# Kernel tuning notes

Hardware: AMD Instinct MI355X
Metric: run time of the kernel (lower is better)

## Reference

```python
import jax, jax.numpy as jnp
import numpy as np

N_NODES = 100000
N_EDGES = 400000
N_GRAPHS = 4096
BN_EPS = 1e-5


def _glorot(key, shape):
    fan_in, fan_out = shape
    lim = np.sqrt(6.0 / (fan_in + fan_out))
    return jax.random.uniform(key, shape, jnp.float32, -lim, lim)


def setup_inputs() -> dict:
    key = jax.random.key(0)
    ks = jax.random.split(key, 16)
    x = jax.random.normal(ks[0], (N_NODES, 373), jnp.float32)
    edge_index = jax.random.randint(ks[1], (2, N_EDGES), 0, N_NODES, jnp.int64)
    batch = jnp.sort(jax.random.randint(ks[2], (N_NODES,), 0, N_GRAPHS, jnp.int64))
    params = {
        # GIN layer 1 MLP: 373->256->256
        'W1a': _glorot(ks[3], (373, 256)), 'b1a': jnp.zeros((256,), jnp.float32),
        'W1b': _glorot(ks[4], (256, 256)), 'b1b': jnp.zeros((256,), jnp.float32),
        'g1': jnp.ones((256,), jnp.float32), 'be1': jnp.zeros((256,), jnp.float32),
        # GIN layer 2 MLP: 256->128->128
        'W2a': _glorot(ks[5], (256, 128)), 'b2a': jnp.zeros((128,), jnp.float32),
        'W2b': _glorot(ks[6], (128, 128)), 'b2b': jnp.zeros((128,), jnp.float32),
        'g2': jnp.ones((128,), jnp.float32), 'be2': jnp.zeros((128,), jnp.float32),
        # GIN layer 3 MLP: 128->64->64
        'W3a': _glorot(ks[7], (128, 64)), 'b3a': jnp.zeros((64,), jnp.float32),
        'W3b': _glorot(ks[8], (64, 64)), 'b3b': jnp.zeros((64,), jnp.float32),
        'g3': jnp.ones((64,), jnp.float32), 'be3': jnp.zeros((64,), jnp.float32),
        # head
        'Wf1': _glorot(ks[9], (64, 16)), 'bf1': jnp.zeros((16,), jnp.float32),
        'Wf2': _glorot(ks[10], (16, 1)), 'bf2': jnp.zeros((1,), jnp.float32),
    }
    return {'x': x, 'edge_index': edge_index, 'batch': batch, **params}


def _gin_conv(x, src, dst, Wa, ba, Wb, bb):
    # sum-aggregate neighbor messages (eps = 0 default in GINConv)
    agg = jax.ops.segment_sum(x[src], dst, num_segments=N_NODES)
    h = x + agg
    h = jax.nn.relu(h @ Wa + ba) @ Wb + bb
    return h


def _batchnorm(x, gamma, beta):
    mu = jnp.mean(x, axis=0)
    var = jnp.var(x, axis=0)
    return (x - mu) * jax.lax.rsqrt(var + BN_EPS) * gamma + beta


def reference(x, edge_index, batch,
              W1a, b1a, W1b, b1b, g1, be1,
              W2a, b2a, W2b, b2b, g2, be2,
              W3a, b3a, W3b, b3b, g3, be3,
              Wf1, bf1, Wf2, bf2):
    src, dst = edge_index[0], edge_index[1]
    h = jax.nn.relu(_gin_conv(x, src, dst, W1a, b1a, W1b, b1b))
    h = _batchnorm(h, g1, be1)
    h = jax.nn.relu(_gin_conv(h, src, dst, W2a, b2a, W2b, b2b))
    h = _batchnorm(h, g2, be2)
    h = jax.nn.relu(_gin_conv(h, src, dst, W3a, b3a, W3b, b3b))
    h = _batchnorm(h, g3, be3)
    # global_add_pool: [N, 64] -> [G, 64]
    pooled = jax.ops.segment_sum(h, batch, num_segments=N_GRAPHS)
    out = jax.nn.relu(pooled @ Wf1 + bf1)
    # dropout omitted (eval mode)
    out = jax.nn.relu(out @ Wf2 + bf2)
    return out.reshape(-1)
```

## Files before the change

### kernel.cpp

```cpp
#include <hip/hip_runtime.h>

#define N_NODES 100000
#define N_EDGES 400000
#define N_GRAPHS 4096
#define BN_EPS 1e-5f
#define DEG_CAP 96

typedef unsigned short ushort_t;
typedef short short8 __attribute__((ext_vector_type(8)));
typedef unsigned short ushort4v __attribute__((ext_vector_type(4)));
typedef unsigned short ushort8v __attribute__((ext_vector_type(8)));
typedef float floatx4 __attribute__((ext_vector_type(4)));

__device__ __forceinline__ ushort_t f2b(float f) {
    union { float f; unsigned u; } v; v.f = f;
    unsigned r = v.u + 0x7fffu + ((v.u >> 16) & 1u);
    return (ushort_t)(r >> 16);
}
__device__ __forceinline__ float b2f(ushort_t b) {
    union { unsigned u; float f; } v; v.u = ((unsigned)b) << 16;
    return v.f;
}

__global__ void k_pad_x(const float* __restrict__ x, ushort_t* __restrict__ xb,
                        int* __restrict__ cursor,
                        const float* __restrict__ W1a, ushort_t* __restrict__ BT1) {
    int t = threadIdx.x;
    if (blockIdx.x >= N_NODES) {
        int b = blockIdx.x - N_NODES;
        int n = b / 3, kc = b % 3;
        int k = kc * 128 + t;
        float v = (k < 373) ? W1a[(long)k * 256 + n] : 0.f;
        BT1[(long)n * 384 + k] = f2b(v);
        return;
    }
    int n = blockIdx.x;
    const float* xr = x + (long)n * 373;
    ushort_t* o = xb + (long)n * 384;
    if (t < 93) {
        float v0 = xr[t * 4 + 0], v1 = xr[t * 4 + 1], v2 = xr[t * 4 + 2], v3 = xr[t * 4 + 3];
        ushort4v s = {f2b(v0), f2b(v1), f2b(v2), f2b(v3)};
        *(ushort4v*)(o + t * 4) = s;
    } else if (t == 93) {
        o[372] = f2b(xr[372]);
        o[373] = 0; o[374] = 0; o[375] = 0;
    } else if (t == 94 || t == 95) {
        ushort4v z = {0, 0, 0, 0};
        *(ushort4v*)(o + 376 + (t - 94) * 4) = z;
    } else if (t == 96) {
        cursor[n] = 0;
    }
}

__global__ void k_fill(const int* __restrict__ src, const int* __restrict__ dst,
                       int* __restrict__ cursor, int* __restrict__ elist) {
    int e = blockIdx.x * blockDim.x + threadIdx.x;
    if (e < N_EDGES) {
        int d = dst[e];
        int slot = atomicAdd(&cursor[d], 1);
        if (slot < DEG_CAP) elist[(long)d * DEG_CAP + slot] = src[e];
    }
}

__global__ void k_prep_scaled(const float* __restrict__ W, const float* __restrict__ scsh,
                              ushort_t* __restrict__ BT, float* __restrict__ biasE,
                              int K, int Kp, int Nn) {
    int n = blockIdx.y;
    int k = blockIdx.x * 128 + threadIdx.x;
    if (k < Kp) {
        float v = (k < K) ? W[(long)k * Nn + n] * scsh[k] : 0.f;
        BT[(long)n * Kp + k] = f2b(v);
    }
    if (blockIdx.x == 0) {
        __shared__ float red[2];
        float s = 0.f;
        for (int kk = threadIdx.x; kk < K; kk += 128) s += scsh[K + kk] * W[(long)kk * Nn + n];
#pragma unroll
        for (int off = 32; off >= 1; off >>= 1) s += __shfl_xor(s, off);
        if ((threadIdx.x & 63) == 0) red[threadIdx.x >> 6] = s;
        __syncthreads();
        if (threadIdx.x == 0) biasE[n] = red[0] + red[1];
    }
}

template<int KP, int TN, bool STATS>
__global__ __launch_bounds__(256) void k_gemm(const ushort_t* __restrict__ A,
                                              const ushort_t* __restrict__ BT,
                                              const float* __restrict__ bias,
                                              ushort_t* __restrict__ C,
                                              float* __restrict__ partials,
                                              int M, int Nn, int relu) {
    __shared__ __align__(16) ushort_t As[128 * 32];
    __shared__ __align__(16) ushort_t Bs[TN * 32];
    __shared__ float swred[STATS ? 4 * 2 * TN : 1];
    const int tid = threadIdx.x;
    const int wave = tid >> 6, lane = tid & 63;
    const int ln = lane & 15, kg = lane >> 4;
    const long rowBase = (long)blockIdx.y * 128;
    const int colBase = blockIdx.x * TN;

    constexpr int RT = (TN == 128) ? 4 : 2;
    const int rowOff = (TN == 128) ? ((wave >> 1) * 64) : (wave * 32);
    const int colOff = (TN == 128) ? ((wave & 1) * 64) : 0;

    const ushort_t* aSrc[2];
#pragma unroll
    for (int i = 0; i < 2; i++) {
        long r = rowBase + i * 64 + (tid >> 2);
        if (r >= M) r = M - 1;
        aSrc[i] = A + r * KP + (tid & 3) * 8;
    }
    const ushort_t* bSrc[TN / 64];
#pragma unroll
    for (int i = 0; i < TN / 64; i++) {
        long cc = colBase + i * 64 + (tid >> 2);
        bSrc[i] = BT + cc * KP + (tid & 3) * 8;
    }
    ushort_t* aDst = As + wave * 512;
    ushort_t* bDst = Bs + wave * 512;

    floatx4 acc[RT][4];
#pragma unroll
    for (int i = 0; i < RT; i++)
#pragma unroll
        for (int j = 0; j < 4; j++) acc[i][j] = (floatx4){0.f, 0.f, 0.f, 0.f};

    for (int k0 = 0; k0 < KP; k0 += 32) {
        __syncthreads();
#pragma unroll
        for (int i = 0; i < 2; i++)
            __builtin_amdgcn_global_load_lds(
                (const __attribute__((address_space(1))) void*)(aSrc[i] + k0),
                (__attribute__((address_space(3))) void*)(aDst + i * 2048), 16, 0, 0);
#pragma unroll
        for (int i = 0; i < TN / 64; i++)
            __builtin_amdgcn_global_load_lds(
                (const __attribute__((address_space(1))) void*)(bSrc[i] + k0),
                (__attribute__((address_space(3))) void*)(bDst + i * 2048), 16, 0, 0);
        __syncthreads();

        short8 afr[RT], bfr[4];
#pragma unroll
        for (int rt = 0; rt < RT; rt++)
            afr[rt] = *(const short8*)&As[(rowOff + rt * 16 + ln) * 32 + kg * 8];
#pragma unroll
        for (int tn = 0; tn < 4; tn++)
            bfr[tn] = *(const short8*)&Bs[(colOff + tn * 16 + ln) * 32 + kg * 8];
#pragma unroll
        for (int rt = 0; rt < RT; rt++)
#pragma unroll
            for (int tn = 0; tn < 4; tn++)
                acc[rt][tn] = __builtin_amdgcn_mfma_f32_16x16x32_bf16(afr[rt], bfr[tn], acc[rt][tn], 0, 0, 0);
    }

    if constexpr (STATS) {
        for (int i = tid; i < 4 * 2 * TN; i += 256) swred[i] = 0.f;
        __syncthreads();
    }

    float sums[4] = {0.f, 0.f, 0.f, 0.f};
    float sqs[4]  = {0.f, 0.f, 0.f, 0.f};
#pragma unroll
    for (int rt = 0; rt < RT; rt++) {
#pragma unroll
        for (int tn = 0; tn < 4; tn++) {
            int gc = colBase + colOff + tn * 16 + ln;
            float bv = bias ? bias[gc] : 0.f;
#pragma unroll
            for (int r = 0; r < 4; r++) {
                long gr = rowBase + rowOff + rt * 16 + kg * 4 + r;
                if (gr < M) {
                    float v = acc[rt][tn][r] + bv;
                    if (relu) v = fmaxf(v, 0.f);
                    ushort_t sb = f2b(v);
                    C[gr * Nn + gc] = sb;
                    if (STATS) {
                        float vb = b2f(sb);
                        sums[tn] += vb;
                        sqs[tn] += vb * vb;
                    }
                }
            }
        }
    }
    if constexpr (STATS) {
#pragma unroll
        for (int tn = 0; tn < 4; tn++) {
            float s = sums[tn], q = sqs[tn];
            s += __shfl_xor(s, 16); q += __shfl_xor(q, 16);
            s += __shfl_xor(s, 32); q += __shfl_xor(q, 32);
            if (kg == 0) {
                int c = colOff + tn * 16 + ln;
                swred[wave * 2 * TN + c] = s;
                swred[wave * 2 * TN + TN + c] = q;
            }
        }
        __syncthreads();
        const int by = blockIdx.y;
        const int gyd = gridDim.y;
        for (int c = tid; c < TN; c += 256) {
            float ssum = 0.f, ssq = 0.f;
#pragma unroll
            for (int w = 0; w < 4; w++) {
                ssum += swred[w * 2 * TN + c];
                ssq  += swred[w * 2 * TN + TN + c];
            }
            long gc = colBase + c;
            partials[gc * gyd + by] = ssum;
            partials[((long)Nn + gc) * gyd + by] = ssq;
        }
    }
}

template<int KP, int TN>
__global__ __launch_bounds__(256, 4) void k_gemm_agg(const ushort_t* __restrict__ y,
                                                  const int* __restrict__ cursor,
                                                  const int* __restrict__ elist,
                                                  const float* __restrict__ badd,
                                                  const ushort_t* __restrict__ BT,
                                                  const float* __restrict__ bias,
                                                  ushort_t* __restrict__ C,
                                                  float* __restrict__ partials,
                                                  int M, int Nn) {
    __shared__ __align__(16) ushort_t Af[128 * KP];
    __shared__ __align__(16) ushort_t Bs[TN * 32];
    float* swred = (float*)Af;
    const int tid = threadIdx.x;
    const int wave = tid >> 6, lane = tid & 63;
    const int ln = lane & 15, kg = lane >> 4;
    const long rowBase = (long)blockIdx.y * 128;
    constexpr int CPR = KP / 8;
    constexpr int TPR = CPR;
    constexpr int RPS = 256 / TPR;

    {
        const int lr = tid / TPR;
        const int ck = tid % TPR;
        const int c0 = ck * 8;
        float bd[8];
#pragma unroll
        for (int j = 0; j < 8; j++) bd[j] = badd[c0 + j];
        for (int s = 0; s < 128; s += RPS) {
            int r = s + lr;
            long gr = rowBase + r; if (gr >= M) gr = M - 1;
            int cnt = cursor[gr]; if (cnt > DEG_CAP) cnt = DEG_CAP;
            const int* el = elist + gr * DEG_CAP;
            int4 e0 = *(const int4*)el;
            int4 e1 = *(const int4*)(el + 4);
            int ids[8] = {e0.x, e0.y, e0.z, e0.w, e1.x, e1.y, e1.z, e1.w};
            ushort8v sv = *(const ushort8v*)(y + gr * KP + c0);
            ushort8v rr[8];
#pragma unroll
            for (int i = 0; i < 8; i++)
                if (i < cnt) rr[i] = *(const ushort8v*)(y + (long)ids[i] * KP + c0);
            float av[8];
#pragma unroll
            for (int j = 0; j < 8; j++) av[j] = b2f(sv[j]);
#pragma unroll
            for (int i = 0; i < 8; i++)
                if (i < cnt) {
#pragma unroll
                    for (int j = 0; j < 8; j++) av[j] += b2f(rr[i][j]);
                }
            for (int i = 8; i < cnt; i++) {
                ushort8v u = *(const ushort8v*)(y + (long)el[i] * KP + c0);
#pragma unroll
                for (int j = 0; j < 8; j++) av[j] += b2f(u[j]);
            }
            ushort8v ov;
#pragma unroll
            for (int j = 0; j < 8; j++) ov[j] = f2b(fmaxf(av[j] + bd[j], 0.f));
            int cks = ck ^ (r & (CPR - 1));
            *(ushort8v*)&Af[r * KP + cks * 8] = ov;
        }
    }

    constexpr int RT = (TN == 128) ? 4 : 2;
    const int rowOff = (TN == 128) ? ((wave >> 1) * 64) : (wave * 32);
    const int colOff = (TN == 128) ? ((wave & 1) * 64) : 0;
    const ushort_t* bSrc[TN / 64];
#pragma unroll
    for (int i = 0; i < TN / 64; i++) {
        long cc = i * 64 + (tid >> 2);
        bSrc[i] = BT + cc * KP + (tid & 3) * 8;
    }
    ushort_t* bDst = Bs + wave * 512;

    floatx4 acc[RT][4];
#pragma unroll
    for (int i = 0; i < RT; i++)
#pragma unroll
        for (int j = 0; j < 4; j++) acc[i][j] = (floatx4){0.f, 0.f, 0.f, 0.f};

    for (int k0 = 0; k0 < KP; k0 += 32) {
        __syncthreads();
#pragma unroll
        for (int i = 0; i < TN / 64; i++)
            __builtin_amdgcn_global_load_lds(
                (const __attribute__((address_space(1))) void*)(bSrc[i] + k0),
                (__attribute__((address_space(3))) void*)(bDst + i * 2048), 16, 0, 0);
        __syncthreads();

        short8 afr[RT], bfr[4];
#pragma unroll
        for (int rt = 0; rt < RT; rt++) {
            int row = rowOff + rt * 16 + ln;
            int cks = ((k0 >> 3) + kg) ^ (row & (CPR - 1));
            afr[rt] = *(const short8*)&Af[row * KP + cks * 8];
        }
#pragma unroll
        for (int tn = 0; tn < 4; tn++)
            bfr[tn] = *(const short8*)&Bs[(colOff + tn * 16 + ln) * 32 + kg * 8];
#pragma unroll
        for (int rt = 0; rt < RT; rt++)
#pragma unroll
            for (int tn = 0; tn < 4; tn++)
                acc[rt][tn] = __builtin_amdgcn_mfma_f32_16x16x32_bf16(afr[rt], bfr[tn], acc[rt][tn], 0, 0, 0);
    }

    __syncthreads();
    for (int i = tid; i < 4 * 2 * TN; i += 256) swred[i] = 0.f;
    __syncthreads();

    float sums[4] = {0.f, 0.f, 0.f, 0.f};
    float sqs[4]  = {0.f, 0.f, 0.f, 0.f};
#pragma unroll
    for (int rt = 0; rt < RT; rt++) {
#pragma unroll
        for (int tn = 0; tn < 4; tn++) {
            int gc = colOff + tn * 16 + ln;
            float bv = bias[gc];
#pragma unroll
            for (int r = 0; r < 4; r++) {
                long gr = rowBase + rowOff + rt * 16 + kg * 4 + r;
                if (gr < M) {
                    float v = fmaxf(acc[rt][tn][r] + bv, 0.f);
                    ushort_t sb = f2b(v);
                    C[gr * Nn + gc] = sb;
                    float vb = b2f(sb);
                    sums[tn] += vb;
                    sqs[tn] += vb * vb;
                }
            }
        }
    }
#pragma unroll
    for (int tn = 0; tn < 4; tn++) {
        float s = sums[tn], q = sqs[tn];
        s += __shfl_xor(s, 16); q += __shfl_xor(q, 16);
        s += __shfl_xor(s, 32); q += __shfl_xor(q, 32);
        if (kg == 0) {
            int c = colOff + tn * 16 + ln;
            swred[wave * 2 * TN + c] = s;
            swred[wave * 2 * TN + TN + c] = q;
        }
    }
    __syncthreads();
    const int by = blockIdx.y;
    const int gyd = gridDim.y;
    for (int c = tid; c < TN; c += 256) {
        float ssum = 0.f, ssq = 0.f;
#pragma unroll
        for (int w = 0; w < 4; w++) {
            ssum += swred[w * 2 * TN + c];
            ssq  += swred[w * 2 * TN + TN + c];
        }
        partials[(long)c * gyd + by] = ssum;
        partials[((long)Nn + c) * gyd + by] = ssq;
    }
}

template<int D>
__global__ void k_aggregate(const ushort_t* __restrict__ y, const int* __restrict__ cursor,
                            const int* __restrict__ elist, const float* __restrict__ badd,
                            ushort_t* __restrict__ out, int nblk,
                            const float* __restrict__ Wn, ushort_t* __restrict__ BTn,
                            int KWn, int NWn) {
    int t = threadIdx.x;
    if ((int)blockIdx.x >= nblk) {
        int b = blockIdx.x - nblk;
        int nk = KWn >> 6;
        int n = b / nk, kc = b - n * nk;
        int k = kc * 64 + t;
        BTn[(long)n * KWn + k] = f2b(Wn[(long)k * NWn + n]);
        return;
    }
    const int CG = D / 4;
    const int NPB = 64 / CG;
    int n = blockIdx.x * NPB + t / CG;
    int c = (t % CG) * 4;
    if (n >= N_NODES) return;
    int cnt = cursor[n];
    if (cnt > DEG_CAP) cnt = DEG_CAP;
    const int* el = elist + (long)n * DEG_CAP;
    int4 e0 = *(const int4*)el;
    int4 e1 = *(const int4*)(el + 4);
    int ids[8] = {e0.x, e0.y, e0.z, e0.w, e1.x, e1.y, e1.z, e1.w};
    ushort4v sv = *(const ushort4v*)(y + (long)n * D + c);
    ushort4v rr[8];
#pragma unroll
    for (int i = 0; i < 8; i++)
        if (i < cnt) rr[i] = *(const ushort4v*)(y + (long)ids[i] * D + c);
    float t0 = b2f(sv.x), t1 = b2f(sv.y), t2 = b2f(sv.z), t3 = b2f(sv.w);
#pragma unroll
    for (int i = 0; i < 8; i++)
        if (i < cnt) {
            t0 += b2f(rr[i].x); t1 += b2f(rr[i].y); t2 += b2f(rr[i].z); t3 += b2f(rr[i].w);
        }
    for (int i = 8; i < cnt; i++) {
        ushort4v u = *(const ushort4v*)(y + (long)el[i] * D + c);
        t0 += b2f(u.x); t1 += b2f(u.y); t2 += b2f(u.z); t3 += b2f(u.w);
    }
    t0 = fmaxf(t0 + badd[c + 0], 0.f);
    t1 = fmaxf(t1 + badd[c + 1], 0.f);
    t2 = fmaxf(t2 + badd[c + 2], 0.f);
    t3 = fmaxf(t3 + badd[c + 3], 0.f);
    ushort4v o = {f2b(t0), f2b(t1), f2b(t2), f2b(t3)};
    *(ushort4v*)(out + (long)n * D + c) = o;
}

__global__ void k_bn(const float* __restrict__ partials, int gy,
                     const float* __restrict__ gamma, const float* __restrict__ beta,
                     float* __restrict__ scsh, int K,
                     const float* __restrict__ Wn, ushort_t* __restrict__ BTn,
                     int KWn, int NWn) {
    int b = blockIdx.x;
    int t = threadIdx.x;
    if (b >= K) {
        int p = b - K;
        int nk = KWn >> 6;
        int n = p / nk, kc = p - n * nk;
        int k = kc * 64 + t;
        BTn[(long)n * KWn + k] = f2b(Wn[(long)k * NWn + n]);
        return;
    }
    const float* ps = partials + (long)b * gy;
    const float* pq = partials + (long)(K + b) * gy;
    float s = 0.f, q = 0.f;
    for (int i = t; i < gy; i += 64) { s += ps[i]; q += pq[i]; }
#pragma unroll
    for (int off = 32; off >= 1; off >>= 1) { s += __shfl_xor(s, off); q += __shfl_xor(q, off); }
    if (t == 0) {
        float invN = 1.0f / (float)N_NODES;
        float mu = s * invN;
        float var = fmaxf(q * invN - mu * mu, 0.f);
        float sc = rsqrtf(var + BN_EPS) * gamma[b];
        scsh[b] = sc;
        scsh[K + b] = beta[b] - mu * sc;
    }
}

__global__ void k_poolhead(const ushort_t* __restrict__ h, const int* __restrict__ batch,
                           const float* __restrict__ scsh,
                           const float* __restrict__ Wf1, const float* __restrict__ bf1,
                           const float* __restrict__ Wf2, const float* __restrict__ bf2,
                           float* __restrict__ out) {
    __shared__ float pl[64];
    __shared__ float hid[16];
    int g = blockIdx.x;
    int c = threadIdx.x;
    int lo = 0, hi = N_NODES;
    while (lo < hi) { int mid = (lo + hi) >> 1; if (batch[mid] < g) lo = mid + 1; else hi = mid; }
    int start = lo;
    hi = N_NODES;
    while (lo < hi) { int mid = (lo + hi) >> 1; if (batch[mid] < g + 1) lo = mid + 1; else hi = mid; }
    int end = lo;
    float s = 0.f;
    for (int r = start; r < end; r++) s += b2f(h[(long)r * 64 + c]);
    pl[c] = s * scsh[c] + scsh[64 + c] * (float)(end - start);
    __syncthreads();
    if (c < 16) {
        float sh = bf1[c];
        for (int j = 0; j < 64; j++) sh += pl[j] * Wf1[j * 16 + c];
        hid[c] = fmaxf(sh, 0.f);
    }
    __syncthreads();
    if (c == 0) {
        float o = bf2[0];
#pragma unroll
        for (int k = 0; k < 16; k++) o += hid[k] * Wf2[k];
        out[g] = fmaxf(o, 0.f);
    }
}

extern "C" void kernel_launch(void* const* d_in, const int* in_sizes, int n_in,
                              void* d_out, int out_size, void* d_ws, size_t ws_size,
                              hipStream_t stream) {
    const float* x    = (const float*)d_in[0];
    const int*  ei    = (const int*)d_in[1];
    const int*  batch = (const int*)d_in[2];
    const float* W1a = (const float*)d_in[3];
    const float* b1a = (const float*)d_in[4];
    const float* W1b = (const float*)d_in[5];
    const float* b1b = (const float*)d_in[6];
    const float* g1  = (const float*)d_in[7];
    const float* be1 = (const float*)d_in[8];
    const float* W2a = (const float*)d_in[9];
    const float* b2a = (const float*)d_in[10];
    const float* W2b = (const float*)d_in[11];
    const float* b2b = (const float*)d_in[12];
    const float* g2  = (const float*)d_in[13];
    const float* be2 = (const float*)d_in[14];
    const float* W3a = (const float*)d_in[15];
    const float* b3a = (const float*)d_in[16];
    const float* W3b = (const float*)d_in[17];
    const float* b3b = (const float*)d_in[18];
    const float* g3  = (const float*)d_in[19];
    const float* be3 = (const float*)d_in[20];
    const float* Wf1 = (const float*)d_in[21];
    const float* bf1 = (const float*)d_in[22];
    const float* Wf2 = (const float*)d_in[23];
    const float* bf2 = (const float*)d_in[24];

    const int N = N_NODES, E = N_EDGES;
    const int* src = ei;
    const int* dst = ei + E;
    const int gy = (N + 127) / 128;

    char* wp = (char*)d_ws;
    auto carve = [&](size_t bytes) {
        char* p = wp;
        wp += (bytes + 255) & ~(size_t)255;
        return (void*)p;
    };
    ushort_t* xb     = (ushort_t*)carve((size_t)N * 384 * 2);
    ushort_t* bufA   = (ushort_t*)carve((size_t)N * 256 * 2);
    ushort_t* bufB   = (ushort_t*)carve((size_t)N * 256 * 2);
    int*      elist  = (int*)carve((size_t)N * DEG_CAP * 4);
    int*      cursor = (int*)carve((size_t)N * 4);
    ushort_t* BT1    = (ushort_t*)carve((size_t)256 * 384 * 2);
    ushort_t* BT2    = (ushort_t*)carve((size_t)256 * 384 * 2);
    float*    scsh   = (float*)carve(512 * 4);
    float*    biasE  = (float*)carve(256 * 4);
    float*    partials = (float*)carve((size_t)2 * 256 * gy * 4);

    dim3 blk(256);

    k_pad_x<<<N + 768, 128, 0, stream>>>(x, xb, cursor, W1a, BT1);
    k_fill<<<(E + 255) / 256, blk, 0, stream>>>(src, dst, cursor, elist);

    k_gemm<384, 128, false><<<dim3(2, gy), blk, 0, stream>>>(xb, BT1, nullptr, bufA, nullptr, N, 256, 0);
    k_aggregate<256><<<N + 1024, 64, 0, stream>>>(bufA, cursor, elist, b1a, bufB, N, W1b, BT2, 256, 256);
    k_gemm<256, 128, true><<<dim3(2, gy), blk, 0, stream>>>(bufB, BT2, b1b, bufA, partials, N, 256, 1);
    k_bn<<<256 + 256, 64, 0, stream>>>(partials, gy, g1, be1, scsh, 256, W2b, BT2, 128, 128);

    k_prep_scaled<<<dim3(2, 128), 128, 0, stream>>>(W2a, scsh, BT1, biasE, 256, 256, 128);
    k_gemm<256, 128, false><<<dim3(1, gy), blk, 0, stream>>>(bufA, BT1, biasE, bufB, nullptr, N, 128, 0);
    k_gemm_agg<128, 128><<<dim3(1, gy), blk, 0, stream>>>(bufB, cursor, elist, b2a, BT2, b2b, bufA, partials, N, 128);
    k_bn<<<128 + 64, 64, 0, stream>>>(partials, gy, g2, be2, scsh, 128, W3b, BT2, 64, 64);

    k_prep_scaled<<<dim3(1, 64), 128, 0, stream>>>(W3a, scsh, BT1, biasE, 128, 128, 64);
    k_gemm<128, 64, false><<<dim3(1, gy), blk, 0, stream>>>(bufA, BT1, biasE, bufB, nullptr, N, 64, 0);
    k_gemm_agg<64, 64><<<dim3(1, gy), blk, 0, stream>>>(bufB, cursor, elist, b3a, BT2, b3b, bufA, partials, N, 64);
    k_bn<<<64, 64, 0, stream>>>(partials, gy, g3, be3, scsh, 64, nullptr, nullptr, 64, 64);

    k_poolhead<<<N_GRAPHS, 64, 0, stream>>>(bufA, batch, scsh, Wf1, bf1, Wf2, bf2, (float*)d_out);
}
```

Baseline: 627.4 us.

## Fuse fp32-to-bf16 conversion of x into first GEMM and widen N tile

Removes the separate padding/conversion pass that wrote a bf16 copy of x. The first GEMM now reads fp32 x directly, converts to bf16 into padded shared memory, and computes all 256 output columns per block. The layer-1 second GEMM also moves to a 256-wide tile so each A tile is loaded once instead of twice. This saves a full write and re-read of the converted input, but the A loads are now scalar, unaligned fp32 reads (row stride 373) done synchronously, and the larger accumulator arrays raise register pressure and may lower occupancy.

```diff
diff --git a/kernel.cpp b/kernel.cpp
--- a/kernel.cpp
+++ b/kernel.cpp
@@ -22,34 +22,20 @@
     return v.f;
 }
 
-__global__ void k_pad_x(const float* __restrict__ x, ushort_t* __restrict__ xb,
-                        int* __restrict__ cursor,
+__global__ void k_prep0(int* __restrict__ cursor,
                         const float* __restrict__ W1a, ushort_t* __restrict__ BT1) {
     int t = threadIdx.x;
-    if (blockIdx.x >= N_NODES) {
-        int b = blockIdx.x - N_NODES;
-        int n = b / 3, kc = b % 3;
-        int k = kc * 128 + t;
-        float v = (k < 373) ? W1a[(long)k * 256 + n] : 0.f;
-        BT1[(long)n * 384 + k] = f2b(v);
+    int b = blockIdx.x;
+    if (b < 782) {
+        int i = b * 128 + t;
+        if (i < N_NODES) cursor[i] = 0;
         return;
     }
-    int n = blockIdx.x;
-    const float* xr = x + (long)n * 373;
-    ushort_t* o = xb + (long)n * 384;
-    if (t < 93) {
-        float v0 = xr[t * 4 + 0], v1 = xr[t * 4 + 1], v2 = xr[t * 4 + 2], v3 = xr[t * 4 + 3];
-        ushort4v s = {f2b(v0), f2b(v1), f2b(v2), f2b(v3)};
-        *(ushort4v*)(o + t * 4) = s;
-    } else if (t == 93) {
-        o[372] = f2b(xr[372]);
-        o[373] = 0; o[374] = 0; o[375] = 0;
-    } else if (t == 94 || t == 95) {
-        ushort4v z = {0, 0, 0, 0};
-        *(ushort4v*)(o + 376 + (t - 94) * 4) = z;
-    } else if (t == 96) {
-        cursor[n] = 0;
-    }
+    b -= 782;
+    int n = b / 3, kc = b % 3;
+    int k = kc * 128 + t;
+    float v = (k < 373) ? W1a[(long)k * 256 + n] : 0.f;
+    BT1[(long)n * 384 + k] = f2b(v);
 }
 
 __global__ void k_fill(const int* __restrict__ src, const int* __restrict__ dst,
@@ -80,6 +66,87 @@
         if ((threadIdx.x & 63) == 0) red[threadIdx.x >> 6] = s;
         __syncthreads();
         if (threadIdx.x == 0) biasE[n] = red[0] + red[1];
+    }
+}
+
+__global__ __launch_bounds__(256) void k_gemm_x(const float* __restrict__ x,
+                                                const ushort_t* __restrict__ BT,
+                                                ushort_t* __restrict__ C, int M) {
+    __shared__ __align__(16) ushort_t As[128 * 40];
+    __shared__ __align__(16) ushort_t Bs[256 * 32];
+    const int tid = threadIdx.x;
+    const int wave = tid >> 6, lane = tid & 63;
+    const int ln = lane & 15, kg = lane >> 4;
+    const long rowBase = (long)blockIdx.x * 128;
+    const int rowOff = (wave >> 1) * 64;
+    const int colOff = (wave & 1) * 128;
+
+    const int sr = tid >> 1;
+    const int sc0 = (tid & 1) * 16;
+    long gr = rowBase + sr; if (gr >= M) gr = M - 1;
+    const float* xr = x + gr * 373;
+
+    const ushort_t* bSrc[4];
+#pragma unroll
+    for (int i = 0; i < 4; i++) {
+        long cc = i * 64 + (tid >> 2);
+        bSrc[i] = BT + cc * 384 + (tid & 3) * 8;
+    }
+    ushort_t* bDst = Bs + wave * 512;
+
+    floatx4 acc[4][8];
+#pragma unroll
+    for (int i = 0; i < 4; i++)
+#pragma unroll
+        for (int j = 0; j < 8; j++) acc[i][j] = (floatx4){0.f, 0.f, 0.f, 0.f};
+
+    for (int k0 = 0; k0 < 384; k0 += 32) {
+        __syncthreads();
+        ushort8v o0, o1;
+#pragma unroll
+        for (int j = 0; j < 8; j++) {
+            int c = k0 + sc0 + j;
+            o0[j] = f2b((c < 373) ? xr[c] : 0.f);
+        }
+#pragma unroll
+        for (int j = 0; j < 8; j++) {
+            int c = k0 + sc0 + 8 + j;
+            o1[j] = f2b((c < 373) ? xr[c] : 0.f);
+        }
+        *(ushort8v*)&As[sr * 40 + sc0] = o0;
+        *(ushort8v*)&As[sr * 40 + sc0 + 8] = o1;
+#pragma unroll
+        for (int i = 0; i < 4; i++)
+            __builtin_amdgcn_global_load_lds(
+                (const __attribute__((address_space(1))) void*)(bSrc[i] + k0),
+                (__attribute__((address_space(3))) void*)(bDst + i * 2048), 16, 0, 0);
+        __syncthreads();
+
+        short8 afr[4], bfr[8];
+#pragma unroll
+        for (int rt = 0; rt < 4; rt++)
+            afr[rt] = *(const short8*)&As[(rowOff + rt * 16 + ln) * 40 + kg * 8];
+#pragma unroll
+        for (int ct = 0; ct < 8; ct++)
+            bfr[ct] = *(const short8*)&Bs[(colOff + ct * 16 + ln) * 32 + kg * 8];
+#pragma unroll
+        for (int rt = 0; rt < 4; rt++)
+#pragma unroll
+            for (int ct = 0; ct < 8; ct++)
+                acc[rt][ct] = __builtin_amdgcn_mfma_f32_16x16x32_bf16(afr[rt], bfr[ct], acc[rt][ct], 0, 0, 0);
+    }
+
+#pragma unroll
+    for (int rt = 0; rt < 4; rt++) {
+#pragma unroll
+        for (int ct = 0; ct < 8; ct++) {
+            int gc = colOff + ct * 16 + ln;
+#pragma unroll
+            for (int r = 0; r < 4; r++) {
+                long g2 = rowBase + rowOff + rt * 16 + kg * 4 + r;
+                if (g2 < M) C[g2 * 256 + gc] = f2b(acc[rt][ct][r]);
+            }
+        }
     }
 }
 
@@ -99,9 +166,10 @@
     const long rowBase = (long)blockIdx.y * 128;
     const int colBase = blockIdx.x * TN;
 
-    constexpr int RT = (TN == 128) ? 4 : 2;
-    const int rowOff = (TN == 128) ? ((wave >> 1) * 64) : (wave * 32);
-    const int colOff = (TN == 128) ? ((wave & 1) * 64) : 0;
+    constexpr int RT = (TN == 64) ? 2 : 4;
+    constexpr int CT = (TN == 256) ? 8 : 4;
+    const int rowOff = (TN == 64) ? (wave * 32) : ((wave >> 1) * 64);
+    const int colOff = (TN == 64) ? 0 : ((wave & 1) * (CT * 16));
 
     const ushort_t* aSrc[2];
 #pragma unroll
@@ -119,11 +187,11 @@
     ushort_t* aDst = As + wave * 512;
     ushort_t* bDst = Bs + wave * 512;
 
-    floatx4 acc[RT][4];
+    floatx4 acc[RT][CT];
 #pragma unroll
     for (int i = 0; i < RT; i++)
 #pragma unroll
-        for (int j = 0; j < 4; j++) acc[i][j] = (floatx4){0.f, 0.f, 0.f, 0.f};
+        for (int j = 0; j < CT; j++) acc[i][j] = (floatx4){0.f, 0.f, 0.f, 0.f};
 
     for (int k0 = 0; k0 < KP; k0 += 32) {
         __syncthreads();
@@ -139,17 +207,17 @@
                 (__attribute__((address_space(3))) void*)(bDst + i * 2048), 16, 0, 0);
         __syncthreads();
 
-        short8 afr[RT], bfr[4];
+        short8 afr[RT], bfr[CT];
 #pragma unroll
         for (int rt = 0; rt < RT; rt++)
             afr[rt] = *(const short8*)&As[(rowOff + rt * 16 + ln) * 32 + kg * 8];
 #pragma unroll
-        for (int tn = 0; tn < 4; tn++)
+        for (int tn = 0; tn < CT; tn++)
             bfr[tn] = *(const short8*)&Bs[(colOff + tn * 16 + ln) * 32 + kg * 8];
 #pragma unroll
         for (int rt = 0; rt < RT; rt++)
 #pragma unroll
-            for (int tn = 0; tn < 4; tn++)
+            for (int tn = 0; tn < CT; tn++)
                 acc[rt][tn] = __builtin_amdgcn_mfma_f32_16x16x32_bf16(afr[rt], bfr[tn], acc[rt][tn], 0, 0, 0);
     }
 
@@ -158,12 +226,13 @@
         __syncthreads();
     }
 
-    float sums[4] = {0.f, 0.f, 0.f, 0.f};
-    float sqs[4]  = {0.f, 0.f, 0.f, 0.f};
+    float sums[CT], sqs[CT];
+#pragma unroll
+    for (int tn = 0; tn < CT; tn++) { sums[tn] = 0.f; sqs[tn] = 0.f; }
 #pragma unroll
     for (int rt = 0; rt < RT; rt++) {
 #pragma unroll
-        for (int tn = 0; tn < 4; tn++) {
+        for (int tn = 0; tn < CT; tn++) {
             int gc = colBase + colOff + tn * 16 + ln;
             float bv = bias ? bias[gc] : 0.f;
 #pragma unroll
@@ -185,7 +254,7 @@
     }
     if constexpr (STATS) {
 #pragma unroll
-        for (int tn = 0; tn < 4; tn++) {
+        for (int tn = 0; tn < CT; tn++) {
             float s = sums[tn], q = sqs[tn];
             s += __shfl_xor(s, 16); q += __shfl_xor(q, 16);
             s += __shfl_xor(s, 32); q += __shfl_xor(q, 32);
@@ -523,7 +592,6 @@
         wp += (bytes + 255) & ~(size_t)255;
         return (void*)p;
     };
-    ushort_t* xb     = (ushort_t*)carve((size_t)N * 384 * 2);
     ushort_t* bufA   = (ushort_t*)carve((size_t)N * 256 * 2);
     ushort_t* bufB   = (ushort_t*)carve((size_t)N * 256 * 2);
     int*      elist  = (int*)carve((size_t)N * DEG_CAP * 4);
@@ -536,12 +604,12 @@
 
     dim3 blk(256);
 
-    k_pad_x<<<N + 768, 128, 0, stream>>>(x, xb, cursor, W1a, BT1);
+    k_prep0<<<782 + 768, 128, 0, stream>>>(cursor, W1a, BT1);
     k_fill<<<(E + 255) / 256, blk, 0, stream>>>(src, dst, cursor, elist);
 
-    k_gemm<384, 128, false><<<dim3(2, gy), blk, 0, stream>>>(xb, BT1, nullptr, bufA, nullptr, N, 256, 0);
+    k_gemm_x<<<gy, blk, 0, stream>>>(x, BT1, bufA, N);
     k_aggregate<256><<<N + 1024, 64, 0, stream>>>(bufA, cursor, elist, b1a, bufB, N, W1b, BT2, 256, 256);
-    k_gemm<256, 128, true><<<dim3(2, gy), blk, 0, stream>>>(bufB, BT2, b1b, bufA, partials, N, 256, 1);
+    k_gemm<256, 256, true><<<dim3(1, gy), blk, 0, stream>>>(bufB, BT2, b1b, bufA, partials, N, 256, 1);
     k_bn<<<256 + 256, 64, 0, stream>>>(partials, gy, g1, be1, scsh, 256, W2b, BT2, 128, 128);
 
     k_prep_scaled<<<dim3(2, 128), 128, 0, stream>>>(W2a, scsh, BT1, biasE, 256, 256, 128);
```

After: 702.2 us. +11.9%, slower.
